# Performance work log

Measured on AMD Instinct MI355X. Metric: run time of the kernel, lower is better.

## Reference

```python
import jax, jax.numpy as jnp
import numpy as np

DIM = 512


def setup_inputs() -> dict:
    key = jax.random.key(0)
    ks = jax.random.split(key, 6)
    b, c, h, w = 8, DIM, 64, 64
    x = jax.random.normal(ks[0], (b, c, h, w), dtype=jnp.float32)
    # complex Linear(dim, 3*dim, bias=False): real weight applied to real & imag parts
    w_qkv = jax.random.normal(ks[1], (3 * c, c), dtype=jnp.float32) * (1.0 / np.sqrt(c))
    w_gate = jax.random.normal(ks[2], (c, c), dtype=jnp.float32) * (1.0 / np.sqrt(c))
    b_gate = jax.random.normal(ks[3], (c,), dtype=jnp.float32) * 0.01
    w_proj = jax.random.normal(ks[4], (c, c), dtype=jnp.float32) * (1.0 / np.sqrt(c))
    b_proj = jax.random.normal(ks[5], (c,), dtype=jnp.float32) * 0.01
    return {"x": x, "w_qkv": w_qkv, "w_gate": w_gate, "b_gate": b_gate,
            "w_proj": w_proj, "b_proj": b_proj}


def reference(x, w_qkv, w_gate, b_gate, w_proj, b_proj):
    b, c, h, w = x.shape
    n = h * w
    xf = jnp.transpose(x, (0, 2, 3, 1))  # b,h,w,c
    # gate: SiLU(Linear(x)) on spatial tokens
    t = jax.nn.silu(xf.reshape(b, n, c) @ w_gate.T + b_gate)  # b,n,c
    # rfft2 over spatial dims, orthonormal
    X = jnp.fft.rfft2(xf, axes=(1, 2), norm="ortho")  # b,h,w//2+1,c complex64
    # complex Linear == real weight applied to real and imag parts independently
    qkv = jnp.einsum("bhwc,dc->bhwd", X, w_qkv.astype(X.dtype))  # b,h,w_r,3c
    q, k, v = jnp.split(qkv, 3, axis=-1)
    attn = jnp.conj(q) * k
    attn = jnp.fft.irfft2(attn, s=(h, w), axes=(1, 2), norm="ortho")  # real b,h,w,c
    # softmax over the n = h*w spatial positions, per channel
    attn = jax.nn.softmax(attn.reshape(b, n, c), axis=1).reshape(b, h, w, c)
    # NOTE: this rfft2 uses torch default norm (backward, no scaling) — faithful
    A = jnp.fft.rfft2(attn, axes=(1, 2))
    y = jnp.conj(A) * v
    y = jnp.fft.irfft2(y, s=(h, w), axes=(1, 2), norm="ortho")  # b,h,w,c real
    y = y.reshape(b, n, c) * t
    y = y @ w_proj.T + b_proj  # proj (dropout p=0 is identity)
    return jnp.transpose(y.reshape(b, h, w, c), (0, 3, 1, 2))  # b,c,h,w
```

## Files before the change

kernel.cpp:

```cpp
#include <hip/hip_runtime.h>
#include <hip/hip_bf16.h>


#define BB 8
#define CC 512
#define HH 64
#define SS 4096
#define WR 33
#define PP 2112

#define TWOPI_64 0.09817477042468103f

typedef float f32x4 __attribute__((ext_vector_type(4)));
typedef __bf16 bf16x8 __attribute__((ext_vector_type(8)));
typedef unsigned short ushort;
typedef ushort ushort8 __attribute__((ext_vector_type(8)));

#define QKV_HI 0
#define QKV_LO 786432
#define GATE_HI 1572864
#define GATE_LO 2097152
#define PROJ_HI 2621440
#define PROJ_LO 3145728

#define TWF_OFF 0
#define TWH0_OFF 12288
#define TWH1_OFF 47104
#define TWH2_OFF 81920
#define TWI_OFF 116736
#define TW_USHORTS 126976

__device__ __forceinline__ void split2(float x, ushort& h, ushort& l) {
  unsigned bx = __builtin_bit_cast(unsigned, x);
  h = (ushort)(bx >> 16);
  float hf = __builtin_bit_cast(float, bx & 0xffff0000u);
  float lf = x - hf;
  l = (ushort)(__builtin_bit_cast(unsigned, lf) >> 16);
}

__device__ __forceinline__ void gll16(const void* src, void* lds_dst) {
  __builtin_amdgcn_global_load_lds(
      (const __attribute__((address_space(1))) unsigned int*)src,
      (__attribute__((address_space(3))) unsigned int*)lds_dst, 16, 0, 0);
}

#define MFMA16(a, b, c) __builtin_amdgcn_mfma_f32_16x16x32_bf16(a, b, c, 0, 0, 0)

__device__ __forceinline__ void pack8(const float* f, bf16x8& hi, bf16x8& lo) {
  ushort8 hs, ls;
#pragma unroll
  for (int j = 0; j < 8; ++j) { ushort h, l; split2(f[j], h, l); hs[j] = h; ls[j] = l; }
  hi = __builtin_bit_cast(bf16x8, hs);
  lo = __builtin_bit_cast(bf16x8, ls);
}

__global__ __launch_bounds__(256) void prep_w(
    const float* __restrict__ wqkv, const float* __restrict__ wg,
    const float* __restrict__ wp, ushort* __restrict__ planes) {
  int i = blockIdx.x * 256 + threadIdx.x;
  float v; ushort *hp, *lp;
  if (i < 786432) {
    v = wqkv[i]; hp = planes + QKV_HI + i; lp = planes + QKV_LO + i;
  } else if (i < 1048576) {
    int j = i - 786432;
    v = wg[j]; hp = planes + GATE_HI + j; lp = planes + GATE_LO + j;
  } else {
    int j = i - 1048576;
    v = wp[j]; hp = planes + PROJ_HI + j; lp = planes + PROJ_LO + j;
  }
  ushort h, l; split2(v, h, l);
  *hp = h; *lp = l;
}

__global__ __launch_bounds__(256) void prep_tw(ushort* __restrict__ tw) {
  int i = blockIdx.x * 256 + threadIdx.x;
  if (i >= 62592) return;
  float val = 0.f; int base, plane, e;
  if (i < 5760) {
    e = i; base = TWF_OFF; plane = 5760;
    int n = e / 72, k = e % 72;
    if (n < 66 && k < 64) {
      int kw = n >> 1;
      float s, c; sincosf(TWOPI_64 * (float)((k * kw) & 63), &s, &c);
      val = (n & 1) ? -s : c;
    }
  } else if (i < 57984) {
    int j = i - 5760; int v = j / 17408; e = j % 17408;
    base = TWH0_OFF + v * 34816; plane = 17408;
    float sgn = (v == 1) ? 1.f : -1.f;
    float scale = (v == 0) ? (1.f / 64.f) : 1.f;
    int n = e / 136, k = e % 136;
    if (k < 128) {
      int kh = n >> 1, q = n & 1, h = k >> 1, p = k & 1;
      float s, c; sincosf(TWOPI_64 * (float)((h * kh) & 63), &s, &c);
      val = (p == q) ? c : ((q == 1) ? sgn * s : -sgn * s);
      val *= scale;
    }
  } else {
    e = i - 57984; base = TWI_OFF; plane = 4608;
    int n = e / 72, k = e % 72;
    if (k < 64) {
      int kk = k >> 1, p = k & 1;
      float w = (kk == 0) ? 1.f : 2.f;
      float s, c; sincosf(TWOPI_64 * (float)((n * kk) & 63), &s, &c);
      val = (p ? -s : c) * w * (1.f / 64.f);
    }
  }
  ushort h, l; split2(val, h, l);
  tw[base + e] = h; tw[base + plane + e] = l;
}

template <int MODE>
__global__ __launch_bounds__(256) void gemm_real(
    const float* __restrict__ act,
    const ushort* __restrict__ w_hi, const ushort* __restrict__ w_lo,
    const float* __restrict__ bias, float* __restrict__ outp) {
  __shared__ float raw[32 * 64];
  __shared__ ushort planeH[64 * 32];
  __shared__ ushort planeL[64 * 32];
  int b = blockIdx.z;
  int m0 = blockIdx.x * 64;
  int d0 = blockIdx.y * 64;
  int tid = threadIdx.x;
  int lane = tid & 63, wid = tid >> 6;
  int fr = lane & 15, fq = lane >> 4;
  int wm = wid & 1, wd = wid >> 1;
  int co = tid >> 6, tm = tid & 63;
  const float* actb = act + (size_t)b * CC * SS + m0;

  f32x4 acc[2][2] = {};

  for (int k0 = 0; k0 < CC; k0 += 32) {
#pragma unroll
    for (int i = 0; i < 2; ++i) {
      int e0 = (i * 256 + tid) * 4;
      int c = e0 >> 6, m = e0 & 63;
      gll16(actb + (size_t)(k0 + c) * SS + m, raw + (i * 256 + (tid & 192)) * 4);
    }
    __syncthreads();
    {
      ushort h[8], l[8];
#pragma unroll
      for (int j = 0; j < 8; ++j) split2(raw[(co * 8 + j) * 64 + tm], h[j], l[j]);
      int ch = ((co ^ (tm & 3)) * 8);
      ushort8 vh, vl;
#pragma unroll
      for (int j = 0; j < 8; ++j) { vh[j] = h[j]; vl[j] = l[j]; }
      *reinterpret_cast<ushort8*>(&planeH[tm * 32 + ch]) = vh;
      *reinterpret_cast<ushort8*>(&planeL[tm * 32 + ch]) = vl;
    }
    __syncthreads();
    bf16x8 wfh[2], wfl[2], afh[2], afl[2];
#pragma unroll
    for (int dt = 0; dt < 2; ++dt) {
      int d = d0 + wd * 32 + dt * 16 + fr;
      size_t wo = (size_t)d * CC + k0 + fq * 8;
      wfh[dt] = *reinterpret_cast<const bf16x8*>(&w_hi[wo]);
      wfl[dt] = *reinterpret_cast<const bf16x8*>(&w_lo[wo]);
    }
#pragma unroll
    for (int mt = 0; mt < 2; ++mt) {
      int m = wm * 32 + mt * 16 + fr;
      int ch = (fq ^ (m & 3)) * 8;
      afh[mt] = *reinterpret_cast<const bf16x8*>(&planeH[m * 32 + ch]);
      afl[mt] = *reinterpret_cast<const bf16x8*>(&planeL[m * 32 + ch]);
    }
#pragma unroll
    for (int mt = 0; mt < 2; ++mt)
#pragma unroll
      for (int dt = 0; dt < 2; ++dt) {
        acc[mt][dt] = MFMA16(afh[mt], wfh[dt], acc[mt][dt]);
        acc[mt][dt] = MFMA16(afh[mt], wfl[dt], acc[mt][dt]);
        acc[mt][dt] = MFMA16(afl[mt], wfh[dt], acc[mt][dt]);
      }
  }
#pragma unroll
  for (int mt = 0; mt < 2; ++mt)
#pragma unroll
    for (int dt = 0; dt < 2; ++dt) {
      int d = d0 + wd * 32 + dt * 16 + fr;
      float bs = bias[d];
      size_t ob = ((size_t)b * CC + d) * SS + m0 + wm * 32 + mt * 16 + fq * 4;
#pragma unroll
      for (int r = 0; r < 4; ++r) {
        float z = acc[mt][dt][r] + bs;
        if (MODE == 0) z = z / (1.f + __expf(-z));
        outp[ob + r] = z;
      }
    }
}

template <int MODE>
__global__ __launch_bounds__(256) void gemm_cplx(
    const float2* __restrict__ X,
    const ushort* __restrict__ w1_hi, const ushort* __restrict__ w1_lo,
    const ushort* __restrict__ w2_hi, const ushort* __restrict__ w2_lo,
    float2* __restrict__ io) {
  __shared__ float raw[32 * 128];
  __shared__ ushort pRH[64 * 32];
  __shared__ ushort pRL[64 * 32];
  __shared__ ushort pIH[64 * 32];
  __shared__ ushort pIL[64 * 32];
  int b = blockIdx.z;
  int m0 = blockIdx.x * 64;
  int d0 = blockIdx.y * 64;
  int tid = threadIdx.x;
  int lane = tid & 63, wid = tid >> 6;
  int fr = lane & 15, fq = lane >> 4;
  int wm = wid & 1, wd = wid >> 1;
  int co = tid >> 6, tm = tid & 63;
  const float* actf = (const float*)(X + (size_t)b * CC * PP + m0);

  f32x4 acc[2][2][MODE == 0 ? 4 : 2] = {};

  for (int k0 = 0; k0 < CC; k0 += 32) {
#pragma unroll
    for (int i = 0; i < 4; ++i) {
      int e0 = (i * 256 + tid) * 4;
      int c = e0 >> 7, r128 = e0 & 127;
      gll16(actf + (size_t)(k0 + c) * PP * 2 + r128,
            raw + (i * 256 + (tid & 192)) * 4);
    }
    __syncthreads();
    {
      const float2* raw2 = (const float2*)raw;
      ushort rh[8], rl[8], ih[8], il[8];
#pragma unroll
      for (int j = 0; j < 8; ++j) {
        float2 v = raw2[(co * 8 + j) * 64 + tm];
        split2(v.x, rh[j], rl[j]);
        split2(v.y, ih[j], il[j]);
      }
      int ch = ((co ^ (tm & 3)) * 8);
      ushort8 vrh, vrl, vih, vil;
#pragma unroll
      for (int j = 0; j < 8; ++j) { vrh[j] = rh[j]; vrl[j] = rl[j]; vih[j] = ih[j]; vil[j] = il[j]; }
      *reinterpret_cast<ushort8*>(&pRH[tm * 32 + ch]) = vrh;
      *reinterpret_cast<ushort8*>(&pRL[tm * 32 + ch]) = vrl;
      *reinterpret_cast<ushort8*>(&pIH[tm * 32 + ch]) = vih;
      *reinterpret_cast<ushort8*>(&pIL[tm * 32 + ch]) = vil;
    }
    __syncthreads();
    bf16x8 w1h[2], w1l[2], w2h[2], w2l[2];
    bf16x8 arh[2], arl[2], aih[2], ail[2];
#pragma unroll
    for (int dt = 0; dt < 2; ++dt) {
      int d = d0 + wd * 32 + dt * 16 + fr;
      size_t wo = (size_t)d * CC + k0 + fq * 8;
      w1h[dt] = *reinterpret_cast<const bf16x8*>(&w1_hi[wo]);
      w1l[dt] = *reinterpret_cast<const bf16x8*>(&w1_lo[wo]);
      if (MODE == 0) {
        w2h[dt] = *reinterpret_cast<const bf16x8*>(&w2_hi[wo]);
        w2l[dt] = *reinterpret_cast<const bf16x8*>(&w2_lo[wo]);
      }
    }
#pragma unroll
    for (int mt = 0; mt < 2; ++mt) {
      int m = wm * 32 + mt * 16 + fr;
      int ch = (fq ^ (m & 3)) * 8;
      arh[mt] = *reinterpret_cast<const bf16x8*>(&pRH[m * 32 + ch]);
      arl[mt] = *reinterpret_cast<const bf16x8*>(&pRL[m * 32 + ch]);
      aih[mt] = *reinterpret_cast<const bf16x8*>(&pIH[m * 32 + ch]);
      ail[mt] = *reinterpret_cast<const bf16x8*>(&pIL[m * 32 + ch]);
    }
#pragma unroll
    for (int mt = 0; mt < 2; ++mt)
#pragma unroll
      for (int dt = 0; dt < 2; ++dt) {
        acc[mt][dt][0] = MFMA16(arh[mt], w1h[dt], acc[mt][dt][0]);
        acc[mt][dt][0] = MFMA16(arh[mt], w1l[dt], acc[mt][dt][0]);
        acc[mt][dt][0] = MFMA16(arl[mt], w1h[dt], acc[mt][dt][0]);
        acc[mt][dt][1] = MFMA16(aih[mt], w1h[dt], acc[mt][dt][1]);
        acc[mt][dt][1] = MFMA16(aih[mt], w1l[dt], acc[mt][dt][1]);
        acc[mt][dt][1] = MFMA16(ail[mt], w1h[dt], acc[mt][dt][1]);
        if (MODE == 0) {
          acc[mt][dt][2] = MFMA16(arh[mt], w2h[dt], acc[mt][dt][2]);
          acc[mt][dt][2] = MFMA16(arh[mt], w2l[dt], acc[mt][dt][2]);
          acc[mt][dt][2] = MFMA16(arl[mt], w2h[dt], acc[mt][dt][2]);
          acc[mt][dt][3] = MFMA16(aih[mt], w2h[dt], acc[mt][dt][3]);
          acc[mt][dt][3] = MFMA16(aih[mt], w2l[dt], acc[mt][dt][3]);
          acc[mt][dt][3] = MFMA16(ail[mt], w2h[dt], acc[mt][dt][3]);
        }
      }
  }
#pragma unroll
  for (int mt = 0; mt < 2; ++mt)
#pragma unroll
    for (int dt = 0; dt < 2; ++dt) {
      int d = d0 + wd * 32 + dt * 16 + fr;
      size_t ob = ((size_t)b * CC + d) * PP + m0 + wm * 32 + mt * 16 + fq * 4;
#pragma unroll
      for (int r = 0; r < 4; ++r) {
        if (MODE == 0) {
          float qr = acc[mt][dt][0][r], qi = acc[mt][dt][1][r];
          float kr = acc[mt][dt][2][r], ki = acc[mt][dt][3][r];
          io[ob + r] = make_float2(qr * kr + qi * ki, qr * ki - qi * kr);
        } else {
          float vr = acc[mt][dt][0][r], vi = acc[mt][dt][1][r];
          float2 a = io[ob + r];
          io[ob + r] = make_float2(a.x * vr + a.y * vi, a.x * vi - a.y * vr);
        }
      }
    }
}

__global__ __launch_bounds__(256) void dftw_fwd(
    const float* __restrict__ in, float* __restrict__ outf,
    const ushort* __restrict__ tw) {
  __shared__ __align__(16) ushort B[12288];
  int tid = threadIdx.x;
  int lane = tid & 63, wid = tid >> 6;
  int fr = lane & 15, fq = lane >> 4;
#pragma unroll
  for (int i = 0; i < 6; ++i)
    gll16((const char*)tw + (i * 256 + tid) * 16,
          (char*)B + (i * 256 + (tid & 192)) * 16);
  __syncthreads();
  bf16x8 bh[5][2], bl[5][2];
#pragma unroll
  for (int nt = 0; nt < 5; ++nt)
#pragma unroll
    for (int ks = 0; ks < 2; ++ks) {
      int o = (nt * 16 + fr) * 72 + ks * 32 + fq * 8;
      bh[nt][ks] = *reinterpret_cast<const bf16x8*>(&B[o]);
      bl[nt][ks] = *reinterpret_cast<const bf16x8*>(&B[5760 + o]);
    }
  for (int chunk = blockIdx.x; chunk < 4096; chunk += gridDim.x) {
    int m0 = chunk * 64 + wid * 16;
    const float* rowp = in + (size_t)(m0 + fr) * 64;
    f32x4 acc[5] = {};
#pragma unroll
    for (int ks = 0; ks < 2; ++ks) {
      float4 v0 = *reinterpret_cast<const float4*>(rowp + ks * 32 + fq * 8);
      float4 v1 = *reinterpret_cast<const float4*>(rowp + ks * 32 + fq * 8 + 4);
      float f[8] = {v0.x, v0.y, v0.z, v0.w, v1.x, v1.y, v1.z, v1.w};
      bf16x8 ah, al; pack8(f, ah, al);
#pragma unroll
      for (int nt = 0; nt < 5; ++nt) {
        acc[nt] = MFMA16(ah, bh[nt][ks], acc[nt]);
        acc[nt] = MFMA16(ah, bl[nt][ks], acc[nt]);
        acc[nt] = MFMA16(al, bh[nt][ks], acc[nt]);
      }
    }
#pragma unroll
    for (int nt = 0; nt < 5; ++nt) {
      int n = nt * 16 + fr;
      if (n < 66) {
#pragma unroll
        for (int r = 0; r < 4; ++r) {
          int m = m0 + fq * 4 + r;
          outf[(size_t)m * 66 + n] = acc[nt][r];
        }
      }
    }
  }
}

__global__ __launch_bounds__(256) void dfth(
    float* __restrict__ io, const ushort* __restrict__ tw) {
  __shared__ __align__(16) ushort B[34816];
  int tid = threadIdx.x;
  int lane = tid & 63, wid = tid >> 6;
  int fr = lane & 15, fq = lane >> 4;
#pragma unroll
  for (int i = 0; i < 17; ++i)
    gll16((const char*)tw + (i * 256 + tid) * 16,
          (char*)B + (i * 256 + (tid & 192)) * 16);
  __syncthreads();
  for (int chunk = blockIdx.x; chunk < 2112; chunk += gridDim.x) {
    int m0 = chunk * 64 + wid * 16;
    int rg = m0 + fr;
    int bc = rg / 33, kw = rg - bc * 33;
    const float* colp = io + ((size_t)bc * PP + kw) * 2;
    bf16x8 ah[4], al[4];
#pragma unroll
    for (int ks = 0; ks < 4; ++ks) {
      float f[8];
#pragma unroll
      for (int e = 0; e < 4; ++e) {
        float2 v = *reinterpret_cast<const float2*>(
            colp + (size_t)(ks * 16 + fq * 4 + e) * WR * 2);
        f[2 * e] = v.x; f[2 * e + 1] = v.y;
      }
      pack8(f, ah[ks], al[ks]);
    }
    f32x4 acc[8] = {};
#pragma unroll
    for (int ks = 0; ks < 4; ++ks)
#pragma unroll
      for (int nt = 0; nt < 8; ++nt) {
        int o = (nt * 16 + fr) * 136 + ks * 32 + fq * 8;
        bf16x8 wh = *reinterpret_cast<const bf16x8*>(&B[o]);
        bf16x8 wl = *reinterpret_cast<const bf16x8*>(&B[17408 + o]);
        acc[nt] = MFMA16(ah[ks], wh, acc[nt]);
        acc[nt] = MFMA16(ah[ks], wl, acc[nt]);
        acc[nt] = MFMA16(al[ks], wh, acc[nt]);
      }
#pragma unroll
    for (int r = 0; r < 4; ++r) {
      int m = m0 + fq * 4 + r;
      int bc2 = m / 33, kw2 = m - bc2 * 33;
      float* outp = io + ((size_t)bc2 * PP + kw2) * 2;
#pragma unroll
      for (int nt = 0; nt < 8; ++nt) {
        int n = nt * 16 + fr;
        int kh = n >> 1, q = n & 1;
        outp[(size_t)kh * WR * 2 + q] = acc[nt][r];
      }
    }
  }
}

__global__ __launch_bounds__(256) void dftw_inv(
    const float* __restrict__ inf, float* __restrict__ out,
    const float* __restrict__ tmul, const ushort* __restrict__ tw) {
  __shared__ __align__(16) ushort B[10240];
  int tid = threadIdx.x;
  int lane = tid & 63, wid = tid >> 6;
  int fr = lane & 15, fq = lane >> 4;
#pragma unroll
  for (int i = 0; i < 5; ++i)
    gll16((const char*)tw + (i * 256 + tid) * 16,
          (char*)B + (i * 256 + (tid & 192)) * 16);
  __syncthreads();
  bf16x8 bh[4][2], bl[4][2];
#pragma unroll
  for (int nt = 0; nt < 4; ++nt)
#pragma unroll
    for (int ks = 0; ks < 2; ++ks) {
      int o = (nt * 16 + fr) * 72 + ks * 32 + fq * 8;
      bh[nt][ks] = *reinterpret_cast<const bf16x8*>(&B[o]);
      bl[nt][ks] = *reinterpret_cast<const bf16x8*>(&B[4608 + o]);
    }
  for (int chunk = blockIdx.x; chunk < 4096; chunk += gridDim.x) {
    int m0 = chunk * 64 + wid * 16;
    const float* rowp = inf + (size_t)(m0 + fr) * 66;
    f32x4 acc[4] = {};
#pragma unroll
    for (int ks = 0; ks < 2; ++ks) {
      float f[8];
#pragma unroll
      for (int e = 0; e < 4; ++e) {
        float2 v = *reinterpret_cast<const float2*>(rowp + ks * 32 + fq * 8 + 2 * e);
        f[2 * e] = v.x; f[2 * e + 1] = v.y;
      }
      bf16x8 ah, al; pack8(f, ah, al);
#pragma unroll
      for (int nt = 0; nt < 4; ++nt) {
        acc[nt] = MFMA16(ah, bh[nt][ks], acc[nt]);
        acc[nt] = MFMA16(ah, bl[nt][ks], acc[nt]);
        acc[nt] = MFMA16(al, bh[nt][ks], acc[nt]);
      }
    }
#pragma unroll
    for (int r = 0; r < 4; ++r) {
      int m = m0 + fq * 4 + r;
      float fr32 = inf[(size_t)m * 66 + 64] * (1.f / 64.f);
#pragma unroll
      for (int nt = 0; nt < 4; ++nt) {
        int x = nt * 16 + fr;
        float res = acc[nt][r] + ((x & 1) ? -fr32 : fr32);
        size_t o = (size_t)m * 64 + x;
        if (tmul) res *= tmul[o];
        out[o] = res;
      }
    }
  }
}

__global__ __launch_bounds__(256) void softmax_n(float* __restrict__ a) {
  __shared__ float red[16];
  int bc = blockIdx.x;
  float* p = a + (size_t)bc * SS;
  int t = threadIdx.x;
  float m = -1e30f;
  for (int i = t; i < SS; i += 256) m = fmaxf(m, p[i]);
#pragma unroll
  for (int off = 32; off > 0; off >>= 1) m = fmaxf(m, __shfl_down(m, off));
  if ((t & 63) == 0) red[t >> 6] = m;
  __syncthreads();
  if (t == 0) red[0] = fmaxf(fmaxf(red[0], red[1]), fmaxf(red[2], red[3]));
  __syncthreads();
  m = red[0];
  float s = 0.f;
  for (int i = t; i < SS; i += 256) s += __expf(p[i] - m);
#pragma unroll
  for (int off = 32; off > 0; off >>= 1) s += __shfl_down(s, off);
  if ((t & 63) == 0) red[8 + (t >> 6)] = s;
  __syncthreads();
  if (t == 0) red[4] = red[8] + red[9] + red[10] + red[11];
  __syncthreads();
  float inv = 1.f / red[4];
  for (int i = t; i < SS; i += 256) p[i] = __expf(p[i] - m) * inv;
}

extern "C" void kernel_launch(void* const* d_in, const int* in_sizes, int n_in,
                              void* d_out, int out_size, void* d_ws, size_t ws_size,
                              hipStream_t stream) {
  const float* x      = (const float*)d_in[0];
  const float* w_qkv  = (const float*)d_in[1];
  const float* w_gate = (const float*)d_in[2];
  const float* b_gate = (const float*)d_in[3];
  const float* w_proj = (const float*)d_in[4];
  const float* b_proj = (const float*)d_in[5];
  float* out = (float*)d_out;

  char* ws = (char*)d_ws;
  float*  T  = (float*)ws;
  float2* W0 = (float2*)(ws + 67108864);
  float2* W1 = (float2*)(ws + 136314880);
  ushort* PL = (ushort*)(ws + 205520896);
  ushort* TW = (ushort*)(ws + 212860928);
  float* W0f = (float*)W0;
  float* W1f = (float*)W1;

  dim3 gemmS(SS / 64, CC / 64, BB);
  dim3 gemmP(PP / 64, CC / 64, BB);

  prep_w<<<1310720 / 256, 256, 0, stream>>>(w_qkv, w_gate, w_proj, PL);
  prep_tw<<<245, 256, 0, stream>>>(TW);
  gemm_real<0><<<gemmS, 256, 0, stream>>>(x, PL + GATE_HI, PL + GATE_LO, b_gate, T);
  dftw_fwd<<<1024, 256, 0, stream>>>(x, W0f, TW + TWF_OFF);
  dfth<<<528, 256, 0, stream>>>(W0f, TW + TWH0_OFF);
  gemm_cplx<0><<<gemmP, 256, 0, stream>>>(W0, PL + QKV_HI, PL + QKV_LO,
                                          PL + QKV_HI + CC * CC, PL + QKV_LO + CC * CC, W1);
  dfth<<<528, 256, 0, stream>>>(W1f, TW + TWH1_OFF);
  dftw_inv<<<1024, 256, 0, stream>>>(W1f, out, nullptr, TW + TWI_OFF);
  softmax_n<<<BB * CC, 256, 0, stream>>>(out);
  dftw_fwd<<<1024, 256, 0, stream>>>(out, W1f, TW + TWF_OFF);
  dfth<<<528, 256, 0, stream>>>(W1f, TW + TWH2_OFF);
  gemm_cplx<1><<<gemmP, 256, 0, stream>>>(W0, PL + QKV_HI + 2 * CC * CC, PL + QKV_LO + 2 * CC * CC,
                                          nullptr, nullptr, W1);
  dfth<<<528, 256, 0, stream>>>(W1f, TW + TWH1_OFF);
  dftw_inv<<<1024, 256, 0, stream>>>(W1f, W0f, T, TW + TWI_OFF);
  gemm_real<1><<<gemmS, 256, 0, stream>>>(W0f, PL + PROJ_HI, PL + PROJ_LO, b_proj, out);
}
```

Measured before the change: 1.107 ms.

## Pre-transpose and pre-split activations so GEMMs load bf16 operands directly

Adds transpose kernels that convert channel-major activations into token-major hi/lo bf16 planes once. The GEMMs can then read MFMA operands straight from global memory, with no LDS staging, no per-tile split, and no barriers. The gate GEMM now runs after the inverse DFT and multiplies its SiLU output into the buffer in place, which removes the T buffer. Block indices are remapped so consecutive blocks spread across batches. The cost is extra transpose passes and extra bf16-plane traffic, plus uncached global operand loads inside the GEMM inner loop.

Result: slower. 1.465 ms (+32.3%).

```diff
diff --git a/kernel.cpp b/kernel.cpp
--- a/kernel.cpp
+++ b/kernel.cpp
@@ -19,16 +19,18 @@
 #define QKV_HI 0
 #define QKV_LO 786432
 #define GATE_HI 1572864
-#define GATE_LO 2097152
-#define PROJ_HI 2621440
-#define PROJ_LO 3145728
+#define GATE_LO 1835008
+#define PROJ_HI 2097152
+#define PROJ_LO 2359296
 
 #define TWF_OFF 0
 #define TWH0_OFF 12288
 #define TWH1_OFF 47104
 #define TWH2_OFF 81920
 #define TWI_OFF 116736
-#define TW_USHORTS 126976
+
+#define SPX 8650752
+#define SPG 16777216
 
 __device__ __forceinline__ void split2(float x, ushort& h, ushort& l) {
   unsigned bx = __builtin_bit_cast(unsigned, x);
@@ -110,158 +112,102 @@
   tw[base + e] = h; tw[base + plane + e] = l;
 }
 
+__global__ __launch_bounds__(256) void xpose_cplx(
+    const float2* __restrict__ in, ushort* __restrict__ xp) {
+  __shared__ float2 tile[64][65];
+  int b = blockIdx.z, p0 = blockIdx.x * 64, c0 = blockIdx.y * 64;
+  int tid = threadIdx.x;
+  int cr = tid >> 2, pq = (tid & 3) * 16;
+  const float2* src = in + ((size_t)b * CC + c0 + cr) * PP + p0 + pq;
+#pragma unroll
+  for (int j = 0; j < 16; ++j) tile[cr][pq + j] = src[j];
+  __syncthreads();
+  int pr = tid >> 2, cq = (tid & 3) * 16;
+  ushort8 rh[2], rl[2], ih[2], il[2];
+#pragma unroll
+  for (int g = 0; g < 2; ++g)
+#pragma unroll
+    for (int j = 0; j < 8; ++j) {
+      float2 v = tile[cq + g * 8 + j][pr];
+      ushort h, l;
+      split2(v.x, h, l); rh[g][j] = h; rl[g][j] = l;
+      split2(v.y, h, l); ih[g][j] = h; il[g][j] = l;
+    }
+  size_t ob = ((size_t)b * PP + p0 + pr) * CC + c0 + cq;
+#pragma unroll
+  for (int g = 0; g < 2; ++g) {
+    *reinterpret_cast<ushort8*>(&xp[ob + g * 8]) = rh[g];
+    *reinterpret_cast<ushort8*>(&xp[SPX + ob + g * 8]) = rl[g];
+    *reinterpret_cast<ushort8*>(&xp[2 * SPX + ob + g * 8]) = ih[g];
+    *reinterpret_cast<ushort8*>(&xp[3 * SPX + ob + g * 8]) = il[g];
+  }
+}
+
+__global__ __launch_bounds__(256) void xpose_real(
+    const float* __restrict__ in, ushort* __restrict__ gx) {
+  __shared__ float tile[64][65];
+  int b = blockIdx.z, s0 = blockIdx.x * 64, c0 = blockIdx.y * 64;
+  int tid = threadIdx.x;
+  int cr = tid >> 2, sq = (tid & 3) * 16;
+  const float* src = in + ((size_t)b * CC + c0 + cr) * SS + s0 + sq;
+#pragma unroll
+  for (int j = 0; j < 16; ++j) tile[cr][sq + j] = src[j];
+  __syncthreads();
+  int sr = tid >> 2, cq = (tid & 3) * 16;
+  ushort8 vh[2], vl[2];
+#pragma unroll
+  for (int g = 0; g < 2; ++g)
+#pragma unroll
+    for (int j = 0; j < 8; ++j) {
+      ushort h, l; split2(tile[cq + g * 8 + j][sr], h, l);
+      vh[g][j] = h; vl[g][j] = l;
+    }
+  size_t ob = ((size_t)b * SS + s0 + sr) * CC + c0 + cq;
+#pragma unroll
+  for (int g = 0; g < 2; ++g) {
+    *reinterpret_cast<ushort8*>(&gx[ob + g * 8]) = vh[g];
+    *reinterpret_cast<ushort8*>(&gx[SPG + ob + g * 8]) = vl[g];
+  }
+}
+
 template <int MODE>
-__global__ __launch_bounds__(256) void gemm_real(
-    const float* __restrict__ act,
-    const ushort* __restrict__ w_hi, const ushort* __restrict__ w_lo,
-    const float* __restrict__ bias, float* __restrict__ outp) {
-  __shared__ float raw[32 * 64];
-  __shared__ ushort planeH[64 * 32];
-  __shared__ ushort planeL[64 * 32];
-  int b = blockIdx.z;
-  int m0 = blockIdx.x * 64;
-  int d0 = blockIdx.y * 64;
+__global__ __launch_bounds__(256) void gemm_cplx_direct(
+    const ushort* __restrict__ xp,
+    const ushort* __restrict__ w1_hi, const ushort* __restrict__ w1_lo,
+    const ushort* __restrict__ w2_hi, const ushort* __restrict__ w2_lo,
+    float2* __restrict__ io) {
+  int work = (blockIdx.x & 7) * 264 + (blockIdx.x >> 3);
+  int b = work / 264, rem = work % 264;
+  int m0 = (rem >> 3) * 64, d0 = (rem & 7) * 64;
   int tid = threadIdx.x;
   int lane = tid & 63, wid = tid >> 6;
   int fr = lane & 15, fq = lane >> 4;
   int wm = wid & 1, wd = wid >> 1;
-  int co = tid >> 6, tm = tid & 63;
-  const float* actb = act + (size_t)b * CC * SS + m0;
-
-  f32x4 acc[2][2] = {};
+
+  f32x4 acc[2][2][MODE == 0 ? 4 : 2] = {};
+  size_t arow0 = ((size_t)b * PP + (m0 + wm * 32 + fr)) * CC;
 
   for (int k0 = 0; k0 < CC; k0 += 32) {
-#pragma unroll
-    for (int i = 0; i < 2; ++i) {
-      int e0 = (i * 256 + tid) * 4;
-      int c = e0 >> 6, m = e0 & 63;
-      gll16(actb + (size_t)(k0 + c) * SS + m, raw + (i * 256 + (tid & 192)) * 4);
-    }
-    __syncthreads();
-    {
-      ushort h[8], l[8];
-#pragma unroll
-      for (int j = 0; j < 8; ++j) split2(raw[(co * 8 + j) * 64 + tm], h[j], l[j]);
-      int ch = ((co ^ (tm & 3)) * 8);
-      ushort8 vh, vl;
-#pragma unroll
-      for (int j = 0; j < 8; ++j) { vh[j] = h[j]; vl[j] = l[j]; }
-      *reinterpret_cast<ushort8*>(&planeH[tm * 32 + ch]) = vh;
-      *reinterpret_cast<ushort8*>(&planeL[tm * 32 + ch]) = vl;
-    }
-    __syncthreads();
-    bf16x8 wfh[2], wfl[2], afh[2], afl[2];
+    int ko = k0 + fq * 8;
+    bf16x8 arh[2], arl[2], aih[2], ail[2];
+#pragma unroll
+    for (int mt = 0; mt < 2; ++mt) {
+      size_t o = arow0 + (size_t)mt * 16 * CC + ko;
+      arh[mt] = *reinterpret_cast<const bf16x8*>(&xp[o]);
+      arl[mt] = *reinterpret_cast<const bf16x8*>(&xp[SPX + o]);
+      aih[mt] = *reinterpret_cast<const bf16x8*>(&xp[2 * SPX + o]);
+      ail[mt] = *reinterpret_cast<const bf16x8*>(&xp[3 * SPX + o]);
+    }
+    bf16x8 w1h[2], w1l[2], w2h[2], w2l[2];
 #pragma unroll
     for (int dt = 0; dt < 2; ++dt) {
-      int d = d0 + wd * 32 + dt * 16 + fr;
-      size_t wo = (size_t)d * CC + k0 + fq * 8;
-      wfh[dt] = *reinterpret_cast<const bf16x8*>(&w_hi[wo]);
-      wfl[dt] = *reinterpret_cast<const bf16x8*>(&w_lo[wo]);
-    }
-#pragma unroll
-    for (int mt = 0; mt < 2; ++mt) {
-      int m = wm * 32 + mt * 16 + fr;
-      int ch = (fq ^ (m & 3)) * 8;
-      afh[mt] = *reinterpret_cast<const bf16x8*>(&planeH[m * 32 + ch]);
-      afl[mt] = *reinterpret_cast<const bf16x8*>(&planeL[m * 32 + ch]);
-    }
-#pragma unroll
-    for (int mt = 0; mt < 2; ++mt)
-#pragma unroll
-      for (int dt = 0; dt < 2; ++dt) {
-        acc[mt][dt] = MFMA16(afh[mt], wfh[dt], acc[mt][dt]);
-        acc[mt][dt] = MFMA16(afh[mt], wfl[dt], acc[mt][dt]);
-        acc[mt][dt] = MFMA16(afl[mt], wfh[dt], acc[mt][dt]);
-      }
-  }
-#pragma unroll
-  for (int mt = 0; mt < 2; ++mt)
-#pragma unroll
-    for (int dt = 0; dt < 2; ++dt) {
-      int d = d0 + wd * 32 + dt * 16 + fr;
-      float bs = bias[d];
-      size_t ob = ((size_t)b * CC + d) * SS + m0 + wm * 32 + mt * 16 + fq * 4;
-#pragma unroll
-      for (int r = 0; r < 4; ++r) {
-        float z = acc[mt][dt][r] + bs;
-        if (MODE == 0) z = z / (1.f + __expf(-z));
-        outp[ob + r] = z;
-      }
-    }
-}
-
-template <int MODE>
-__global__ __launch_bounds__(256) void gemm_cplx(
-    const float2* __restrict__ X,
-    const ushort* __restrict__ w1_hi, const ushort* __restrict__ w1_lo,
-    const ushort* __restrict__ w2_hi, const ushort* __restrict__ w2_lo,
-    float2* __restrict__ io) {
-  __shared__ float raw[32 * 128];
-  __shared__ ushort pRH[64 * 32];
-  __shared__ ushort pRL[64 * 32];
-  __shared__ ushort pIH[64 * 32];
-  __shared__ ushort pIL[64 * 32];
-  int b = blockIdx.z;
-  int m0 = blockIdx.x * 64;
-  int d0 = blockIdx.y * 64;
-  int tid = threadIdx.x;
-  int lane = tid & 63, wid = tid >> 6;
-  int fr = lane & 15, fq = lane >> 4;
-  int wm = wid & 1, wd = wid >> 1;
-  int co = tid >> 6, tm = tid & 63;
-  const float* actf = (const float*)(X + (size_t)b * CC * PP + m0);
-
-  f32x4 acc[2][2][MODE == 0 ? 4 : 2] = {};
-
-  for (int k0 = 0; k0 < CC; k0 += 32) {
-#pragma unroll
-    for (int i = 0; i < 4; ++i) {
-      int e0 = (i * 256 + tid) * 4;
-      int c = e0 >> 7, r128 = e0 & 127;
-      gll16(actf + (size_t)(k0 + c) * PP * 2 + r128,
-            raw + (i * 256 + (tid & 192)) * 4);
-    }
-    __syncthreads();
-    {
-      const float2* raw2 = (const float2*)raw;
-      ushort rh[8], rl[8], ih[8], il[8];
-#pragma unroll
-      for (int j = 0; j < 8; ++j) {
-        float2 v = raw2[(co * 8 + j) * 64 + tm];
-        split2(v.x, rh[j], rl[j]);
-        split2(v.y, ih[j], il[j]);
-      }
-      int ch = ((co ^ (tm & 3)) * 8);
-      ushort8 vrh, vrl, vih, vil;
-#pragma unroll
-      for (int j = 0; j < 8; ++j) { vrh[j] = rh[j]; vrl[j] = rl[j]; vih[j] = ih[j]; vil[j] = il[j]; }
-      *reinterpret_cast<ushort8*>(&pRH[tm * 32 + ch]) = vrh;
-      *reinterpret_cast<ushort8*>(&pRL[tm * 32 + ch]) = vrl;
-      *reinterpret_cast<ushort8*>(&pIH[tm * 32 + ch]) = vih;
-      *reinterpret_cast<ushort8*>(&pIL[tm * 32 + ch]) = vil;
-    }
-    __syncthreads();
-    bf16x8 w1h[2], w1l[2], w2h[2], w2l[2];
-    bf16x8 arh[2], arl[2], aih[2], ail[2];
-#pragma unroll
-    for (int dt = 0; dt < 2; ++dt) {
-      int d = d0 + wd * 32 + dt * 16 + fr;
-      size_t wo = (size_t)d * CC + k0 + fq * 8;
+      size_t wo = (size_t)(d0 + wd * 32 + dt * 16 + fr) * CC + ko;
       w1h[dt] = *reinterpret_cast<const bf16x8*>(&w1_hi[wo]);
       w1l[dt] = *reinterpret_cast<const bf16x8*>(&w1_lo[wo]);
       if (MODE == 0) {
         w2h[dt] = *reinterpret_cast<const bf16x8*>(&w2_hi[wo]);
         w2l[dt] = *reinterpret_cast<const bf16x8*>(&w2_lo[wo]);
       }
-    }
-#pragma unroll
-    for (int mt = 0; mt < 2; ++mt) {
-      int m = wm * 32 + mt * 16 + fr;
-      int ch = (fq ^ (m & 3)) * 8;
-      arh[mt] = *reinterpret_cast<const bf16x8*>(&pRH[m * 32 + ch]);
-      arl[mt] = *reinterpret_cast<const bf16x8*>(&pRL[m * 32 + ch]);
-      aih[mt] = *reinterpret_cast<const bf16x8*>(&pIH[m * 32 + ch]);
-      ail[mt] = *reinterpret_cast<const bf16x8*>(&pIL[m * 32 + ch]);
     }
 #pragma unroll
     for (int mt = 0; mt < 2; ++mt)
@@ -304,6 +250,66 @@
     }
 }
 
+template <int MODE>
+__global__ __launch_bounds__(256) void gemm_real_direct(
+    const ushort* __restrict__ gx,
+    const ushort* __restrict__ w_hi, const ushort* __restrict__ w_lo,
+    const float* __restrict__ bias, float* __restrict__ io) {
+  int work = (blockIdx.x & 7) * 512 + (blockIdx.x >> 3);
+  int b = work / 512, rem = work % 512;
+  int m0 = (rem >> 3) * 64, d0 = (rem & 7) * 64;
+  int tid = threadIdx.x;
+  int lane = tid & 63, wid = tid >> 6;
+  int fr = lane & 15, fq = lane >> 4;
+  int wm = wid & 1, wd = wid >> 1;
+
+  f32x4 acc[2][2] = {};
+  size_t arow0 = ((size_t)b * SS + (m0 + wm * 32 + fr)) * CC;
+
+  for (int k0 = 0; k0 < CC; k0 += 32) {
+    int ko = k0 + fq * 8;
+    bf16x8 ah[2], al[2], wh[2], wl[2];
+#pragma unroll
+    for (int mt = 0; mt < 2; ++mt) {
+      size_t o = arow0 + (size_t)mt * 16 * CC + ko;
+      ah[mt] = *reinterpret_cast<const bf16x8*>(&gx[o]);
+      al[mt] = *reinterpret_cast<const bf16x8*>(&gx[SPG + o]);
+    }
+#pragma unroll
+    for (int dt = 0; dt < 2; ++dt) {
+      size_t wo = (size_t)(d0 + wd * 32 + dt * 16 + fr) * CC + ko;
+      wh[dt] = *reinterpret_cast<const bf16x8*>(&w_hi[wo]);
+      wl[dt] = *reinterpret_cast<const bf16x8*>(&w_lo[wo]);
+    }
+#pragma unroll
+    for (int mt = 0; mt < 2; ++mt)
+#pragma unroll
+      for (int dt = 0; dt < 2; ++dt) {
+        acc[mt][dt] = MFMA16(ah[mt], wh[dt], acc[mt][dt]);
+        acc[mt][dt] = MFMA16(ah[mt], wl[dt], acc[mt][dt]);
+        acc[mt][dt] = MFMA16(al[mt], wh[dt], acc[mt][dt]);
+      }
+  }
+#pragma unroll
+  for (int mt = 0; mt < 2; ++mt)
+#pragma unroll
+    for (int dt = 0; dt < 2; ++dt) {
+      int d = d0 + wd * 32 + dt * 16 + fr;
+      float bs = bias[d];
+      size_t ob = ((size_t)b * CC + d) * SS + m0 + wm * 32 + mt * 16 + fq * 4;
+#pragma unroll
+      for (int r = 0; r < 4; ++r) {
+        float z = acc[mt][dt][r] + bs;
+        if (MODE == 0) {
+          float t = z / (1.f + __expf(-z));
+          io[ob + r] *= t;
+        } else {
+          io[ob + r] = z;
+        }
+      }
+    }
+}
+
 __global__ __launch_bounds__(256) void dftw_fwd(
     const float* __restrict__ in, float* __restrict__ outf,
     const ushort* __restrict__ tw) {
@@ -506,32 +512,33 @@
   float* out = (float*)d_out;
 
   char* ws = (char*)d_ws;
-  float*  T  = (float*)ws;
-  float2* W0 = (float2*)(ws + 67108864);
-  float2* W1 = (float2*)(ws + 136314880);
-  ushort* PL = (ushort*)(ws + 205520896);
-  ushort* TW = (ushort*)(ws + 212860928);
-  float* W0f = (float*)W0;
-  float* W1f = (float*)W1;
-
-  dim3 gemmS(SS / 64, CC / 64, BB);
-  dim3 gemmP(PP / 64, CC / 64, BB);
-
-  prep_w<<<1310720 / 256, 256, 0, stream>>>(w_qkv, w_gate, w_proj, PL);
+  float*  W0f = (float*)ws;
+  float2* W0c = (float2*)W0f;
+  float*  W1f = (float*)(ws + 69206016);
+  float2* W1c = (float2*)W1f;
+  ushort* XP  = (ushort*)(ws + 138412032);
+  ushort* GX  = XP;
+  ushort* PL  = (ushort*)(ws + 207618048);
+  ushort* TW  = (ushort*)(ws + 212860928);
+
+  prep_w<<<5120, 256, 0, stream>>>(w_qkv, w_gate, w_proj, PL);
   prep_tw<<<245, 256, 0, stream>>>(TW);
-  gemm_real<0><<<gemmS, 256, 0, stream>>>(x, PL + GATE_HI, PL + GATE_LO, b_gate, T);
   dftw_fwd<<<1024, 256, 0, stream>>>(x, W0f, TW + TWF_OFF);
   dfth<<<528, 256, 0, stream>>>(W0f, TW + TWH0_OFF);
-  gemm_cplx<0><<<gemmP, 256, 0, stream>>>(W0, PL + QKV_HI, PL + QKV_LO,
-                                          PL + QKV_HI + CC * CC, PL + QKV_LO + CC * CC, W1);
+  xpose_cplx<<<dim3(33, 8, 8), 256, 0, stream>>>(W0c, XP);
+  gemm_cplx_direct<0><<<2112, 256, 0, stream>>>(XP, PL + QKV_HI, PL + QKV_LO,
+                                                PL + QKV_HI + 262144, PL + QKV_LO + 262144, W1c);
   dfth<<<528, 256, 0, stream>>>(W1f, TW + TWH1_OFF);
   dftw_inv<<<1024, 256, 0, stream>>>(W1f, out, nullptr, TW + TWI_OFF);
   softmax_n<<<BB * CC, 256, 0, stream>>>(out);
   dftw_fwd<<<1024, 256, 0, stream>>>(out, W1f, TW + TWF_OFF);
   dfth<<<528, 256, 0, stream>>>(W1f, TW + TWH2_OFF);
-  gemm_cplx<1><<<gemmP, 256, 0, stream>>>(W0, PL + QKV_HI + 2 * CC * CC, PL + QKV_LO + 2 * CC * CC,
-                                          nullptr, nullptr, W1);
+  gemm_cplx_direct<1><<<2112, 256, 0, stream>>>(XP, PL + QKV_HI + 524288, PL + QKV_LO + 524288,
+                                                nullptr, nullptr, W1c);
   dfth<<<528, 256, 0, stream>>>(W1f, TW + TWH1_OFF);
-  dftw_inv<<<1024, 256, 0, stream>>>(W1f, W0f, T, TW + TWI_OFF);
-  gemm_real<1><<<gemmS, 256, 0, stream>>>(W0f, PL + PROJ_HI, PL + PROJ_LO, b_proj, out);
-}
+  dftw_inv<<<1024, 256, 0, stream>>>(W1f, W0f, nullptr, TW + TWI_OFF);
+  xpose_real<<<dim3(64, 8, 8), 256, 0, stream>>>(x, GX);
+  gemm_real_direct<0><<<4096, 256, 0, stream>>>(GX, PL + GATE_HI, PL + GATE_LO, b_gate, W0f);
+  xpose_real<<<dim3(64, 8, 8), 256, 0, stream>>>(W0f, GX);
+  gemm_real_direct<1><<<4096, 256, 0, stream>>>(GX, PL + PROJ_HI, PL + PROJ_LO, b_proj, out);
+}
```
